# Optimization experiments

Measured on AMD Instinct MI355X. Metric: run time of the kernel, lower is better.

The kernel has to match this reference:

```python
import jax, jax.numpy as jnp
import numpy as np

NUM_EMBEDDINGS = 2048
EMBEDDING_DIM = 128
BETA = 0.25


def setup_inputs() -> dict:
    key = jax.random.key(0)
    k1, k2 = jax.random.split(key)
    z = jax.random.normal(k1, (64, 32, 32, EMBEDDING_DIM), dtype=jnp.float32)
    # nn.Embedding init: uniform(-1/K, 1/K)
    emb = jax.random.uniform(k2, (NUM_EMBEDDINGS, EMBEDDING_DIM), dtype=jnp.float32,
                             minval=-1.0 / NUM_EMBEDDINGS, maxval=1.0 / NUM_EMBEDDINGS)
    return {"z": z, "emb": emb}


def reference(z, emb):
    beta = BETA
    flat = z.reshape(-1, EMBEDDING_DIM)  # [N, D]
    dist = (jnp.sum(flat * flat, axis=1, keepdims=True)
            - 2.0 * flat @ emb.T
            + jnp.sum(emb * emb, axis=1))
    indices = jnp.argmin(dist, axis=1)  # [N]
    quantized = emb[indices].reshape(z.shape)
    # commitment / codebook loss
    loss = (jnp.mean((jax.lax.stop_gradient(quantized) - z) ** 2)
            + beta * jnp.mean((quantized - jax.lax.stop_gradient(z)) ** 2))
    # straight-through estimator
    quantized_st = z + jax.lax.stop_gradient(quantized - z)
    indices_out = indices.reshape(z.shape[0], -1)
    return quantized_st, indices_out, loss
```

## Files before the change

kernel.cpp:

```cpp
#include <hip/hip_runtime.h>

#define NUM_EMB 2048
#define DIM     128
#define NVEC    65536
#define MARGIN  1.0e-3f
#define CAP     32
#define CHUNK   512
#define NCHUNK  (NUM_EMB / CHUNK)
#define ES      136
#define ZS      132

typedef float  f32x4 __attribute__((ext_vector_type(4)));
typedef short  s16x8 __attribute__((ext_vector_type(8)));

__device__ __forceinline__ ushort f2bf(float f) {
    unsigned u = __float_as_uint(f);
    u = (u + 0x7fffu + ((u >> 16) & 1u)) >> 16;
    return (ushort)u;
}

__device__ __forceinline__ float np_pairwise_sumsq_128(const float* __restrict__ p)
{
    float r[8];
    #pragma unroll
    for (int j = 0; j < 8; ++j) { float v = p[j]; r[j] = __fmul_rn(v, v); }
    #pragma unroll
    for (int i = 8; i < 128; i += 8)
        #pragma unroll
        for (int j = 0; j < 8; ++j) { float v = p[i + j]; r[j] = __fadd_rn(r[j], __fmul_rn(v, v)); }
    float s01 = __fadd_rn(r[0], r[1]);
    float s23 = __fadd_rn(r[2], r[3]);
    float s45 = __fadd_rn(r[4], r[5]);
    float s67 = __fadd_rn(r[6], r[7]);
    return __fadd_rn(__fadd_rn(s01, s23), __fadd_rn(s45, s67));
}

__device__ __forceinline__ float dot_seg(const float4* __restrict__ zp,
                                         const float4* __restrict__ ep,
                                         int seg, float dot)
{
    float4 e[8], zz[8];
    #pragma unroll
    for (int i = 0; i < 8; ++i) { e[i] = ep[seg * 8 + i]; zz[i] = zp[seg * 8 + i]; }
    #pragma unroll
    for (int i = 0; i < 8; ++i) {
        dot = fmaf(zz[i].x, e[i].x, dot);
        dot = fmaf(zz[i].y, e[i].y, dot);
        dot = fmaf(zz[i].z, e[i].z, dot);
        dot = fmaf(zz[i].w, e[i].w, dot);
    }
    return dot;
}

__global__ __launch_bounds__(256)
void prep_kernel(const float* __restrict__ emb,
                 float* __restrict__ enorm,
                 float* __restrict__ accum,
                 ushort* __restrict__ emb_bf)
{
    int g = blockIdx.x * 256 + threadIdx.x;
    if (g == 0) *accum = 0.0f;

    float4 v = ((const float4*)emb)[g];
    ushort4 b;
    b.x = f2bf(v.x); b.y = f2bf(v.y); b.z = f2bf(v.z); b.w = f2bf(v.w);
    ((ushort4*)emb_bf)[g] = b;

    if (g < NUM_EMB)
        enorm[g] = np_pairwise_sumsq_128(emb + (size_t)g * DIM);
}

__global__ __launch_bounds__(1024, 4)
void approx_kernel(const float* __restrict__ z,
                   const ushort* __restrict__ emb_bf,
                   const float* __restrict__ enorm,
                   unsigned* __restrict__ cand_cnt,
                   ushort* __restrict__ cand)
{
    __shared__ __align__(16) ushort eS[CHUNK * ES];
    __shared__ float cS[CHUNK];
    __shared__ float vS[16][32];
    __shared__ unsigned cntS[256];

    const int tid  = threadIdx.x;
    const int w    = tid >> 6;
    const int lane = tid & 63;
    const int col  = lane & 15;
    const int quad = lane >> 4;
    const int rg   = w >> 1;
    const int ch   = w & 1;
    const int rowbase = blockIdx.x * 256 + rg * 32;

    if (tid < 256) cntS[tid] = 0u;

    s16x8 afrag[2][4];
    #pragma unroll
    for (int mt = 0; mt < 2; ++mt) {
        const float* zr = z + (size_t)(rowbase + mt * 16 + col) * DIM;
        #pragma unroll
        for (int kt = 0; kt < 4; ++kt) {
            const float4* p = (const float4*)(zr + kt * 32 + quad * 8);
            float4 f0 = p[0], f1 = p[1];
            s16x8 a;
            a[0] = (short)f2bf(f0.x); a[1] = (short)f2bf(f0.y);
            a[2] = (short)f2bf(f0.z); a[3] = (short)f2bf(f0.w);
            a[4] = (short)f2bf(f1.x); a[5] = (short)f2bf(f1.y);
            a[6] = (short)f2bf(f1.z); a[7] = (short)f2bf(f1.w);
            afrag[mt][kt] = a;
        }
    }

    const ushort* eH = eS + ch * 256 * ES;
    const float*  cH = cS + ch * 256;

    float vmax[8], thr[8];
    #pragma unroll
    for (int i = 0; i < 8; ++i) { vmax[i] = -3.0e38f; thr[i] = 3.0e38f; }

    for (int vis = 0; vis < NCHUNK; ++vis) {
        if (vis > 0) __syncthreads();

        const uint4* src = (const uint4*)(emb_bf + (size_t)vis * CHUNK * DIM);
        #pragma unroll
        for (int i = 0; i < 8; ++i) {
            int li = i * 1024 + tid;
            int code = li >> 4, fc = li & 15;
            *(uint4*)&eS[code * ES + fc * 8] = src[li];
        }
        if (tid < CHUNK) cS[tid] = -0.5f * enorm[vis * CHUNK + tid];

        if (vis > 0) {
            #pragma unroll
            for (int i = 0; i < 8; ++i) {
                float v = fmaxf(vmax[i], vS[w ^ 1][(i >> 2) * 16 + quad * 4 + (i & 3)]);
                vmax[i] = v;
                thr[i]  = v - 0.5f * MARGIN;
            }
        }
        __syncthreads();

        #pragma unroll 4
        for (int t = 0; t < 16; ++t) {
            s16x8 bfrag[4];
            #pragma unroll
            for (int kt = 0; kt < 4; ++kt)
                bfrag[kt] = *(const s16x8*)&eH[(t * 16 + col) * ES + kt * 32 + quad * 8];

            float h = cH[t * 16 + col];
            f32x4 a0 = {h, h, h, h};
            f32x4 a1 = {h, h, h, h};
            #pragma unroll
            for (int kt = 0; kt < 4; ++kt) {
                a0 = __builtin_amdgcn_mfma_f32_16x16x32_bf16(afrag[0][kt], bfrag[kt], a0, 0, 0, 0);
                a1 = __builtin_amdgcn_mfma_f32_16x16x32_bf16(afrag[1][kt], bfrag[kt], a1, 0, 0, 0);
            }

            #pragma unroll
            for (int r = 0; r < 4; ++r) {
                vmax[r]     = fmaxf(vmax[r],     a0[r]);
                vmax[4 + r] = fmaxf(vmax[4 + r], a1[r]);
            }

            if (vis == 0) {
                #pragma unroll
                for (int i = 0; i < 8; ++i) {
                    float v = vmax[i];
                    v = fmaxf(v, __shfl_xor(v, 1, 64));
                    v = fmaxf(v, __shfl_xor(v, 2, 64));
                    v = fmaxf(v, __shfl_xor(v, 4, 64));
                    v = fmaxf(v, __shfl_xor(v, 8, 64));
                    vmax[i] = v;
                    thr[i]  = v - 0.5f * MARGIN;
                }
            }

            const int code_g = vis * CHUNK + ch * 256 + t * 16 + col;
            #pragma unroll
            for (int r = 0; r < 4; ++r) {
                if (a0[r] >= thr[r]) {
                    int row_l = rg * 32 + quad * 4 + r;
                    unsigned pos = atomicAdd(&cntS[row_l], 1u);
                    if (pos < CAP)
                        cand[(size_t)(blockIdx.x * 256 + row_l) * CAP + pos] = (ushort)code_g;
                }
                if (a1[r] >= thr[4 + r]) {
                    int row_l = rg * 32 + 16 + quad * 4 + r;
                    unsigned pos = atomicAdd(&cntS[row_l], 1u);
                    if (pos < CAP)
                        cand[(size_t)(blockIdx.x * 256 + row_l) * CAP + pos] = (ushort)code_g;
                }
            }
        }

        if (vis > 0) {
            #pragma unroll
            for (int i = 0; i < 8; ++i) {
                float v = vmax[i];
                v = fmaxf(v, __shfl_xor(v, 1, 64));
                v = fmaxf(v, __shfl_xor(v, 2, 64));
                v = fmaxf(v, __shfl_xor(v, 4, 64));
                v = fmaxf(v, __shfl_xor(v, 8, 64));
                vmax[i] = v;
                thr[i]  = v - 0.5f * MARGIN;
            }
        }
        if (col == 0) {
            #pragma unroll
            for (int i = 0; i < 8; ++i)
                vS[w][(i >> 2) * 16 + quad * 4 + (i & 3)] = vmax[i];
        }
    }

    __syncthreads();
    if (tid < 256) cand_cnt[blockIdx.x * 256 + tid] = cntS[tid];
}

__global__ __launch_bounds__(256)
void rerank_kernel(const float* __restrict__ z,
                   const float* __restrict__ emb,
                   const float* __restrict__ enorm,
                   const unsigned* __restrict__ cand_cnt,
                   const ushort* __restrict__ cand,
                   float* __restrict__ out_q,
                   float* __restrict__ out_idx_f,
                   float* __restrict__ accum)
{
    __shared__ float zs[64 * ZS];
    __shared__ float As[64];
    __shared__ int   bidx[64];
    __shared__ int   ovf_list[64];
    __shared__ int   ovf_n;
    __shared__ float rv[4];
    __shared__ int   rvi[4];
    __shared__ float wsum[4];

    const int tid = threadIdx.x;
    const int m0  = blockIdx.x * 64;
    if (tid == 0) ovf_n = 0;

    #pragma unroll
    for (int i = 0; i < 8; ++i) {
        int li = tid + i * 256;
        int m  = li >> 5, dc = li & 31;
        float4 v = ((const float4*)(z + (size_t)(m0 + m) * DIM))[dc];
        *(float4*)&zs[m * ZS + dc * 4] = v;
    }
    __syncthreads();
    if (tid < 64) As[tid] = np_pairwise_sumsq_128(&zs[tid * ZS]);
    __syncthreads();

    const int row_l = tid >> 2;
    const int sub   = tid & 3;
    const int row_g = m0 + row_l;
    const unsigned cnt = cand_cnt[row_g];
    const float A = As[row_l];
    const float4* zp = (const float4*)&zs[row_l * ZS];

    float bv = 3.0e38f;
    int   bi = 0x7fffffff;

    if (cnt <= CAP) {
        for (unsigned ci = sub; ci < cnt; ci += 4) {
            int j = (int)cand[(size_t)row_g * CAP + ci];
            const float4* ep = (const float4*)(emb + (size_t)j * DIM);
            float dot = 0.0f;
            #pragma unroll
            for (int seg = 0; seg < 4; ++seg) dot = dot_seg(zp, ep, seg, dot);
            float t1 = fmaf(-2.0f, dot, A);
            float s  = __fadd_rn(t1, enorm[j]);
            if (s < bv || (s == bv && j < bi)) { bv = s; bi = j; }
        }
    }
    #pragma unroll
    for (int off = 1; off <= 2; off <<= 1) {
        float v  = __shfl_xor(bv, off, 64);
        int   ix = __shfl_xor(bi, off, 64);
        if (v < bv || (v == bv && ix < bi)) { bv = v; bi = ix; }
    }
    if (sub == 0) {
        if (cnt <= CAP) bidx[row_l] = bi;
        else { int p = atomicAdd(&ovf_n, 1); ovf_list[p] = row_l; }
    }
    __syncthreads();

    const int n_ovf = ovf_n;
    for (int o = 0; o < n_ovf; ++o) {
        const int rl = ovf_list[o];
        const float Ar = As[rl];
        const float4* zp2 = (const float4*)&zs[rl * ZS];
        float bv2 = 3.0e38f;
        int   bi2 = 0x7fffffff;
        for (int jj = 0; jj < 8; ++jj) {
            int j = tid * 8 + jj;
            const float4* ep = (const float4*)(emb + (size_t)j * DIM);
            float dot = 0.0f;
            #pragma unroll
            for (int seg = 0; seg < 4; ++seg) dot = dot_seg(zp2, ep, seg, dot);
            float t1 = fmaf(-2.0f, dot, Ar);
            float s  = __fadd_rn(t1, enorm[j]);
            if (s < bv2) { bv2 = s; bi2 = j; }
        }
        #pragma unroll
        for (int off = 1; off < 64; off <<= 1) {
            float v  = __shfl_xor(bv2, off, 64);
            int   ix = __shfl_xor(bi2, off, 64);
            if (v < bv2 || (v == bv2 && ix < bi2)) { bv2 = v; bi2 = ix; }
        }
        if ((tid & 63) == 0) { rv[tid >> 6] = bv2; rvi[tid >> 6] = bi2; }
        __syncthreads();
        if (tid == 0) {
            float fv = rv[0]; int fi = rvi[0];
            #pragma unroll
            for (int ww = 1; ww < 4; ++ww) {
                if (rv[ww] < fv || (rv[ww] == fv && rvi[ww] < fi)) { fv = rv[ww]; fi = rvi[ww]; }
            }
            bidx[rl] = fi;
        }
        __syncthreads();
    }

    if (tid < 64) out_idx_f[m0 + tid] = (float)bidx[tid];

    float part = 0.0f;
    #pragma unroll
    for (int i = 0; i < 8; ++i) {
        int li = tid + i * 256;
        int m  = li >> 5, dc = li & 31;
        int j  = bidx[m];
        float4 q  = ((const float4*)(emb + (size_t)j * DIM))[dc];
        float4 zv = *(const float4*)&zs[m * ZS + dc * 4];
        float4 o;
        o.x = __fadd_rn(zv.x, __fsub_rn(q.x, zv.x));
        o.y = __fadd_rn(zv.y, __fsub_rn(q.y, zv.y));
        o.z = __fadd_rn(zv.z, __fsub_rn(q.z, zv.z));
        o.w = __fadd_rn(zv.w, __fsub_rn(q.w, zv.w));
        ((float4*)out_q)[(size_t)(m0 + m) * 32 + dc] = o;
        float dx = q.x - zv.x, dy = q.y - zv.y, dz = q.z - zv.z, dw = q.w - zv.w;
        part += dx * dx + dy * dy + dz * dz + dw * dw;
    }
    #pragma unroll
    for (int off = 32; off > 0; off >>= 1)
        part += __shfl_down(part, off, 64);
    if ((tid & 63) == 0) wsum[tid >> 6] = part;
    __syncthreads();
    if (tid == 0) atomicAdd(accum, wsum[0] + wsum[1] + wsum[2] + wsum[3]);
}

__global__ void finalize_kernel(const float* __restrict__ accum,
                                float* __restrict__ out_loss)
{
    *out_loss = 1.25f * (*accum) / 8388608.0f;
}

extern "C" void kernel_launch(void* const* d_in, const int* in_sizes, int n_in,
                              void* d_out, int out_size, void* d_ws, size_t ws_size,
                              hipStream_t stream)
{
    const float* z   = (const float*)d_in[0];
    const float* emb = (const float*)d_in[1];
    float* out = (float*)d_out;

    char*     ws       = (char*)d_ws;
    float*    enorm    = (float*)ws;
    float*    accum    = (float*)(ws + 8192);
    unsigned* cand_cnt = (unsigned*)(ws + 16384);
    ushort*   cand     = (ushort*)(ws + 16384 + 262144);
    ushort*   emb_bf   = (ushort*)(ws + 16384 + 262144 + 4194304);

    prep_kernel   <<<NVEC / 256, 256,  0, stream>>>(emb, enorm, accum, emb_bf);
    approx_kernel <<<NVEC / 256, 1024, 0, stream>>>(z, emb_bf, enorm, cand_cnt, cand);
    rerank_kernel <<<NVEC / 64,  256,  0, stream>>>(z, emb, enorm, cand_cnt, cand,
                                                    out, out + 8388608, accum);
    finalize_kernel<<<1, 1, 0, stream>>>(accum, out + 8388608 + 65536);
}
```

Measured before the change: 259.4 us.

## Rerank candidates with one thread per candidate slot and smaller blocks

The rerank kernel now processes 32 rows per block with 512 threads. It assigns one thread per candidate slot (32 slots per row), replacing the old scheme where 4 threads looped over a row's candidates. Per-slot distances go to shared memory and are reduced with a 16-lane shuffle argmin, which removes the serial candidate loop and load imbalance between rows. The trade-offs are more shared memory traffic and an extra barrier, and the overflow path now runs full-codebook scans with 512 threads per block.

```diff
diff --git a/kernel.cpp b/kernel.cpp
--- a/kernel.cpp
+++ b/kernel.cpp
@@ -9,6 +9,8 @@
 #define NCHUNK  (NUM_EMB / CHUNK)
 #define ES      136
 #define ZS      132
+#define RROWS   32
+#define RTHR    512
 
 typedef float  f32x4 __attribute__((ext_vector_type(4)));
 typedef short  s16x8 __attribute__((ext_vector_type(8)));
@@ -215,7 +217,7 @@
     if (tid < 256) cand_cnt[blockIdx.x * 256 + tid] = cntS[tid];
 }
 
-__global__ __launch_bounds__(256)
+__global__ __launch_bounds__(RTHR, 4)
 void rerank_kernel(const float* __restrict__ z,
                    const float* __restrict__ emb,
                    const float* __restrict__ enorm,
@@ -225,61 +227,72 @@
                    float* __restrict__ out_idx_f,
                    float* __restrict__ accum)
 {
-    __shared__ float zs[64 * ZS];
-    __shared__ float As[64];
-    __shared__ int   bidx[64];
-    __shared__ int   ovf_list[64];
+    __shared__ float zs[RROWS * ZS];
+    __shared__ float sL[RROWS * 32];
+    __shared__ int   jL[RROWS * 32];
+    __shared__ float As[RROWS];
+    __shared__ unsigned cntL[RROWS];
+    __shared__ int   bidx[RROWS];
+    __shared__ int   ovf_list[RROWS];
     __shared__ int   ovf_n;
-    __shared__ float rv[4];
-    __shared__ int   rvi[4];
-    __shared__ float wsum[4];
+    __shared__ float rv[8];
+    __shared__ int   rvi[8];
+    __shared__ float wsum[8];
 
     const int tid = threadIdx.x;
-    const int m0  = blockIdx.x * 64;
+    const int m0  = blockIdx.x * RROWS;
     if (tid == 0) ovf_n = 0;
 
     #pragma unroll
-    for (int i = 0; i < 8; ++i) {
-        int li = tid + i * 256;
+    for (int i = 0; i < 2; ++i) {
+        int li = tid + i * RTHR;
         int m  = li >> 5, dc = li & 31;
         float4 v = ((const float4*)(z + (size_t)(m0 + m) * DIM))[dc];
         *(float4*)&zs[m * ZS + dc * 4] = v;
     }
-    __syncthreads();
-    if (tid < 64) As[tid] = np_pairwise_sumsq_128(&zs[tid * ZS]);
-    __syncthreads();
-
-    const int row_l = tid >> 2;
-    const int sub   = tid & 3;
-    const int row_g = m0 + row_l;
-    const unsigned cnt = cand_cnt[row_g];
-    const float A = As[row_l];
-    const float4* zp = (const float4*)&zs[row_l * ZS];
-
-    float bv = 3.0e38f;
-    int   bi = 0x7fffffff;
-
-    if (cnt <= CAP) {
-        for (unsigned ci = sub; ci < cnt; ci += 4) {
-            int j = (int)cand[(size_t)row_g * CAP + ci];
+    if (tid < RROWS) cntL[tid] = cand_cnt[m0 + tid];
+    __syncthreads();
+    if (tid < RROWS) As[tid] = np_pairwise_sumsq_128(&zs[tid * ZS]);
+    __syncthreads();
+
+    #pragma unroll
+    for (int it = 0; it < 2; ++it) {
+        int slot = tid + it * RTHR;
+        int r  = slot >> 5;
+        int ci = slot & 31;
+        float s = 3.0e38f;
+        int   j = 0x7fffffff;
+        unsigned cnt = cntL[r];
+        if (cnt <= CAP && ci < (int)cnt) {
+            j = (int)cand[(size_t)(m0 + r) * CAP + ci];
             const float4* ep = (const float4*)(emb + (size_t)j * DIM);
+            const float4* zp = (const float4*)&zs[r * ZS];
             float dot = 0.0f;
             #pragma unroll
             for (int seg = 0; seg < 4; ++seg) dot = dot_seg(zp, ep, seg, dot);
-            float t1 = fmaf(-2.0f, dot, A);
-            float s  = __fadd_rn(t1, enorm[j]);
-            if (s < bv || (s == bv && j < bi)) { bv = s; bi = j; }
-        }
-    }
-    #pragma unroll
-    for (int off = 1; off <= 2; off <<= 1) {
-        float v  = __shfl_xor(bv, off, 64);
-        int   ix = __shfl_xor(bi, off, 64);
-        if (v < bv || (v == bv && ix < bi)) { bv = v; bi = ix; }
-    }
-    if (sub == 0) {
-        if (cnt <= CAP) bidx[row_l] = bi;
-        else { int p = atomicAdd(&ovf_n, 1); ovf_list[p] = row_l; }
+            float t1 = fmaf(-2.0f, dot, As[r]);
+            s = __fadd_rn(t1, enorm[j]);
+        }
+        sL[slot] = s;
+        jL[slot] = j;
+    }
+    __syncthreads();
+
+    {
+        int r = tid >> 4, k = tid & 15;
+        float bv = sL[r * 32 + k];       int bi = jL[r * 32 + k];
+        float v2 = sL[r * 32 + 16 + k];  int i2 = jL[r * 32 + 16 + k];
+        if (v2 < bv || (v2 == bv && i2 < bi)) { bv = v2; bi = i2; }
+        #pragma unroll
+        for (int off = 1; off <= 8; off <<= 1) {
+            float v  = __shfl_xor(bv, off, 64);
+            int   ix = __shfl_xor(bi, off, 64);
+            if (v < bv || (v == bv && ix < bi)) { bv = v; bi = ix; }
+        }
+        if (k == 0) {
+            if (cntL[r] <= CAP) bidx[r] = bi;
+            else { int p = atomicAdd(&ovf_n, 1); ovf_list[p] = r; }
+        }
     }
     __syncthreads();
 
@@ -290,8 +303,8 @@
         const float4* zp2 = (const float4*)&zs[rl * ZS];
         float bv2 = 3.0e38f;
         int   bi2 = 0x7fffffff;
-        for (int jj = 0; jj < 8; ++jj) {
-            int j = tid * 8 + jj;
+        for (int jj = 0; jj < 4; ++jj) {
+            int j = tid * 4 + jj;
             const float4* ep = (const float4*)(emb + (size_t)j * DIM);
             float dot = 0.0f;
             #pragma unroll
@@ -311,7 +324,7 @@
         if (tid == 0) {
             float fv = rv[0]; int fi = rvi[0];
             #pragma unroll
-            for (int ww = 1; ww < 4; ++ww) {
+            for (int ww = 1; ww < 8; ++ww) {
                 if (rv[ww] < fv || (rv[ww] == fv && rvi[ww] < fi)) { fv = rv[ww]; fi = rvi[ww]; }
             }
             bidx[rl] = fi;
@@ -319,12 +332,12 @@
         __syncthreads();
     }
 
-    if (tid < 64) out_idx_f[m0 + tid] = (float)bidx[tid];
+    if (tid < RROWS) out_idx_f[m0 + tid] = (float)bidx[tid];
 
     float part = 0.0f;
     #pragma unroll
-    for (int i = 0; i < 8; ++i) {
-        int li = tid + i * 256;
+    for (int i = 0; i < 2; ++i) {
+        int li = tid + i * RTHR;
         int m  = li >> 5, dc = li & 31;
         int j  = bidx[m];
         float4 q  = ((const float4*)(emb + (size_t)j * DIM))[dc];
@@ -343,7 +356,12 @@
         part += __shfl_down(part, off, 64);
     if ((tid & 63) == 0) wsum[tid >> 6] = part;
     __syncthreads();
-    if (tid == 0) atomicAdd(accum, wsum[0] + wsum[1] + wsum[2] + wsum[3]);
+    if (tid == 0) {
+        float t = 0.0f;
+        #pragma unroll
+        for (int ww = 0; ww < 8; ++ww) t += wsum[ww];
+        atomicAdd(accum, t);
+    }
 }
 
 __global__ void finalize_kernel(const float* __restrict__ accum,
@@ -369,7 +387,7 @@
 
     prep_kernel   <<<NVEC / 256, 256,  0, stream>>>(emb, enorm, accum, emb_bf);
     approx_kernel <<<NVEC / 256, 1024, 0, stream>>>(z, emb_bf, enorm, cand_cnt, cand);
-    rerank_kernel <<<NVEC / 64,  256,  0, stream>>>(z, emb, enorm, cand_cnt, cand,
-                                                    out, out + 8388608, accum);
+    rerank_kernel <<<NVEC / RROWS, RTHR, 0, stream>>>(z, emb, enorm, cand_cnt, cand,
+                                                      out, out + 8388608, accum);
     finalize_kernel<<<1, 1, 0, stream>>>(accum, out + 8388608 + 65536);
 }
```

Result: slower. 306.1 us (+18.0%).
